# Performance work log

Hardware: AMD Instinct MI355X
Metric: run time of the kernel (lower is better)

Reference implementation:

```python
import jax, jax.numpy as jnp
import numpy as np

N = 5000
NFEAT = 512
NHID = 64
NHEADS = 8
NCLASS = 40
ALPHA = 0.2  # leaky relu slope
NEG_INF = -9e15


def setup_inputs() -> dict:
    key = jax.random.key(0)
    ks = jax.random.split(key, 12)
    x = jax.random.normal(ks[0], (N, NFEAT), dtype=jnp.float32)
    # binary adjacency, ~32 avg degree, with self loops
    adj = (jax.random.uniform(ks[1], (N, N)) < (32.0 / N)).astype(jnp.float32)
    adj = jnp.maximum(adj, jnp.eye(N, dtype=jnp.float32))
    s = 1.0 / np.sqrt(NFEAT)
    W_h = jax.random.uniform(ks[2], (NHEADS, NFEAT, NHID), minval=-s, maxval=s, dtype=jnp.float32)
    a_h = jax.random.uniform(ks[3], (NHEADS, 2 * NHID), minval=-s, maxval=s, dtype=jnp.float32)
    s2 = 1.0 / np.sqrt(NHID * NHEADS)
    W_o = jax.random.uniform(ks[4], (NHID * NHEADS, NHID), minval=-s2, maxval=s2, dtype=jnp.float32)
    a_o = jax.random.uniform(ks[5], (2 * NHID,), minval=-s2, maxval=s2, dtype=jnp.float32)
    s3 = 1.0 / np.sqrt(NHID)
    fc1_w = jax.random.uniform(ks[6], (NHID, 200), minval=-s3, maxval=s3, dtype=jnp.float32)
    fc1_b = jax.random.uniform(ks[7], (200,), minval=-s3, maxval=s3, dtype=jnp.float32)
    s4 = 1.0 / np.sqrt(200)
    fc2_w = jax.random.uniform(ks[8], (200, NCLASS), minval=-s4, maxval=s4, dtype=jnp.float32)
    fc2_b = jax.random.uniform(ks[9], (NCLASS,), minval=-s4, maxval=s4, dtype=jnp.float32)
    return {"x": x, "adj": adj, "W_h": W_h, "a_h": a_h, "W_o": W_o, "a_o": a_o,
            "fc1_w": fc1_w, "fc1_b": fc1_b, "fc2_w": fc2_w, "fc2_b": fc2_b}


def _masked_attention(e, adj):
    # e: [..., N, N]; mask where adj == 0, then row softmax
    e = jnp.where(adj > 0, e, NEG_INF)
    return jax.nn.softmax(e, axis=-1)


def reference(x, adj, W_h, a_h, W_o, a_o, fc1_w, fc1_b, fc2_w, fc2_b):
    # ---- multi-head GAT layer (concat=True), eval mode (dropout off) ----
    Wh = jnp.einsum('nf,hfo->hno', x, W_h)                 # [H, N, nhid]
    f1 = jnp.einsum('hno,ho->hn', Wh, a_h[:, :NHID])       # [H, N]
    f2 = jnp.einsum('hno,ho->hn', Wh, a_h[:, NHID:])       # [H, N]
    e = jax.nn.leaky_relu(f1[:, :, None] + f2[:, None, :], ALPHA)  # [H, N, N]
    att = _masked_attention(e, adj[None, :, :])
    h = jnp.einsum('hnm,hmo->hno', att, Wh)                # [H, N, nhid]
    h1 = jax.nn.elu(h).transpose(1, 0, 2).reshape(N, NHEADS * NHID)  # concat heads

    # ---- output GAT layer (concat=False) ----
    Wh2 = h1 @ W_o                                         # [N, nhid]
    g1 = Wh2 @ a_o[:NHID]                                  # [N]
    g2 = Wh2 @ a_o[NHID:]                                  # [N]
    e2 = jax.nn.leaky_relu(g1[:, None] + g2[None, :], ALPHA)
    att2 = _masked_attention(e2, adj)
    h2 = att2 @ Wh2                                        # [N, nhid]

    # ---- MLP head ----
    h3 = jax.nn.elu(h2 @ fc1_w + fc1_b)
    return h3 @ fc2_w + fc2_b                              # [N, nclass]
```

## Files before the change

### kernel.cpp

```cpp
#include <hip/hip_runtime.h>

typedef unsigned short u16;
typedef unsigned int u32;
typedef unsigned long long u64;
typedef __bf16 bf16_t;
typedef __bf16 bf16x8 __attribute__((ext_vector_type(8)));
typedef float f32x4 __attribute__((ext_vector_type(4)));
typedef u32 u32x4 __attribute__((ext_vector_type(4)));

#define NN 5000
#define NF 512
#define NH 64
#define HEADS 8
#define NCLS 40
#define CAP 128
#define LRELU 0.2f

#define CVT_BIG 320
#define CVT_GRID (CVT_BIG + 8)
#define BM_BLKS 1250
#define G1_BLKS (79 * HEADS)

__device__ __forceinline__ bool adj_is_bf16(const void* adj) {
    return ((*(const u32*)adj) & 0xFFFFu) != 0u;
}
__device__ __forceinline__ u16 rne_bf16(float f) {
    u32 u = __float_as_uint(f);
    u += 0x7FFFu + ((u >> 16) & 1u);
    return (u16)(u >> 16);
}
__device__ __forceinline__ float up_bf16(u16 h) {
    return __uint_as_float((u32)h << 16);
}
__device__ __forceinline__ u32x4 ntload4(const void* p, int idx) {
    return __builtin_nontemporal_load(((const u32x4*)p) + idx);
}

__global__ __launch_bounds__(256) void cvt(const void* __restrict__ x, const void* __restrict__ W_h,
                                           const void* __restrict__ adj,
                                           const void* a_h, const void* W_o, const void* a_o,
                                           const void* f1w, const void* f1b,
                                           const void* f2w, const void* f2b,
                                           u16* __restrict__ xc, u16* __restrict__ whc,
                                           float* a_hc, float* W_oc, float* a_oc,
                                           float* f1wc, float* f1bc, float* f2wc, float* f2bc) {
    const bool isb = adj_is_bf16(adj);
    const int b = blockIdx.x;
    if (b < CVT_BIG) {
        const int X4 = NN * NF / 4;
        const int T4 = X4 + HEADS * NF * NH / 4;
        for (int i = b * 256 + threadIdx.x; i < T4; i += CVT_BIG * 256) {
            if (i < X4) {
                ushort4 o;
                if (isb) {
                    o = ((const ushort4*)x)[i];
                } else {
                    u32x4 vv = ntload4(x, i);
                    o.x = rne_bf16(__uint_as_float(vv[0])); o.y = rne_bf16(__uint_as_float(vv[1]));
                    o.z = rne_bf16(__uint_as_float(vv[2])); o.w = rne_bf16(__uint_as_float(vv[3]));
                }
                ((ushort4*)xc)[i] = o;
            } else {
                const int iw = i - X4;
                u16 q[4];
                if (isb) {
                    ushort4 vv = ((const ushort4*)W_h)[iw];
                    q[0] = vv.x; q[1] = vv.y; q[2] = vv.z; q[3] = vv.w;
                } else {
                    u32x4 vv = ntload4(W_h, iw);
                    q[0] = rne_bf16(__uint_as_float(vv[0])); q[1] = rne_bf16(__uint_as_float(vv[1]));
                    q[2] = rne_bf16(__uint_as_float(vv[2])); q[3] = rne_bf16(__uint_as_float(vv[3]));
                }
                const int e0 = iw * 4;
                const int h = e0 >> 15;
                const int rem = e0 & 32767;
                const int f = rem >> 6, o0 = rem & 63;
                const int base = (h * 16 + (f >> 5)) * 2048 + ((f >> 3) & 3) * 128 + (f & 7);
                #pragma unroll
                for (int k = 0; k < 4; ++k) {
                    const int o = o0 + k;
                    whc[base + (o >> 4) * 512 + (o & 15) * 8] = q[k];
                }
            }
        }
    } else {
        const int s0 = HEADS * 2 * NH, s1 = HEADS * NH * NH, s2 = 2 * NH,
                  s3 = NH * 200, s4 = 200, s5 = 200 * NCLS, s6 = NCLS;
        const int total = s0 + s1 + s2 + s3 + s4 + s5 + s6;
        for (int i = (b - CVT_BIG) * 256 + threadIdx.x; i < total; i += 8 * 256) {
            const void* src; float* dst; int off = i;
            if (off < s0) { src = a_h; dst = a_hc; }
            else if ((off -= s0) < s1) { src = W_o;  dst = W_oc; }
            else if ((off -= s1) < s2) { src = a_o;  dst = a_oc; }
            else if ((off -= s2) < s3) { src = f1w;  dst = f1wc; }
            else if ((off -= s3) < s4) { src = f1b;  dst = f1bc; }
            else if ((off -= s4) < s5) { src = f2w;  dst = f2wc; }
            else { off -= s5;           src = f2b;  dst = f2bc; }
            dst[off] = isb ? up_bf16(((const u16*)src)[off]) : ((const float*)src)[off];
        }
    }
}

__global__ __launch_bounds__(256) void gemm1_f(const bf16_t* __restrict__ x,
                                               const bf16_t* __restrict__ Wf,
                                               const float* __restrict__ a_h,
                                               const void* __restrict__ adj,
                                               int* __restrict__ nbr, int* __restrict__ deg,
                                               float* __restrict__ Wh,
                                               float* __restrict__ f1,
                                               float* __restrict__ f2) {
    const int lane = threadIdx.x & 63;
    const int wid  = threadIdx.x >> 6;
    const int b = blockIdx.x;

    if (b >= G1_BLKS) {
        const bool isb = adj_is_bf16(adj);
        const int r = (b - G1_BLKS) * 4 + wid;
        u64 my0 = 0ull, my1 = 0ull;
        if (!isb) {
            const float* row = (const float*)adj + (size_t)r * NN;
            #pragma unroll
            for (int pass = 0; pass < 2; ++pass) {
                u32x4 v[10];
                #pragma unroll
                for (int k = 0; k < 10; ++k) {
                    int c = (pass * 10 + k) * 64 + lane;
                    v[k] = (c < 1250) ? ntload4(row, c) : (u32x4){0u, 0u, 0u, 0u};
                }
                #pragma unroll
                for (int k = 0; k < 10; ++k) {
                    int i = pass * 10 + k;
                    #pragma unroll
                    for (int j = 0; j < 4; ++j) {
                        u64 m = __ballot(v[k][j] != 0u);
                        int w = i * 4 + j;
                        if (w == lane)      my0 = m;
                        if (w == lane + 64) my1 = m;
                    }
                }
            }
        } else {
            const u16* row = (const u16*)adj + (size_t)r * NN;
            u32x4 v[10];
            #pragma unroll
            for (int k = 0; k < 10; ++k) {
                int c = k * 64 + lane;
                v[k] = (c < 625) ? ntload4(row, c) : (u32x4){0u, 0u, 0u, 0u};
            }
            #pragma unroll
            for (int k = 0; k < 10; ++k) {
                #pragma unroll
                for (int j = 0; j < 4; ++j) {
                    u64 mlo = __ballot((v[k][j] & 0xFFFFu) != 0u);
                    u64 mhi = __ballot((v[k][j] >> 16) != 0u);
                    int wl = k * 8 + 2 * j, wh = wl + 1;
                    if (wl == lane)      my0 = mlo;
                    if (wl == lane + 64) my1 = mlo;
                    if (wh == lane)      my0 = mhi;
                    if (wh == lane + 64) my1 = mhi;
                }
            }
        }
        int* nrow = nbr + (size_t)r * CAP;
        int pc = __popcll(my0);
        int scan = pc;
        #pragma unroll
        for (int o = 1; o < 64; o <<= 1) {
            int t2 = __shfl_up(scan, o);
            if (lane >= o) scan += t2;
        }
        int off = scan - pc;
        {
            const int w = lane;
            u64 mw = my0;
            while (mw) {
                int bb = __ffsll(mw) - 1;
                mw &= mw - 1;
                int elem = !isb ? ((w >> 2) * 64 + bb) * 4 + (w & 3)
                                : ((w >> 3) * 64 + bb) * 8 + (w & 7);
                if (off < CAP) nrow[off] = elem;
                ++off;
            }
        }
        const int base = __shfl(scan, 63);
        int pc1 = __popcll(my1);
        int scan1 = pc1;
        #pragma unroll
        for (int o = 1; o < 64; o <<= 1) {
            int t2 = __shfl_up(scan1, o);
            if (lane >= o) scan1 += t2;
        }
        int off1 = base + scan1 - pc1;
        {
            const int w = lane + 64;
            u64 mw = my1;
            while (mw) {
                int bb = __ffsll(mw) - 1;
                mw &= mw - 1;
                int elem = !isb ? ((w >> 2) * 64 + bb) * 4 + (w & 3)
                                : ((w >> 3) * 64 + bb) * 8 + (w & 7);
                if (off1 < CAP) nrow[off1] = elem;
                ++off1;
            }
        }
        const int total = base + __shfl(scan1, 63);
        if (lane == 0) deg[r] = total < CAP ? total : CAP;
        return;
    }

    const int rg = b % 79;
    const int h  = b / 79;
    const int quad = lane >> 4;
    const int lr   = lane & 15;
    const int kq   = quad * 8;
    const int nCol = wid * 16 + lr;
    __shared__ float f1s[4][64], f2s[4][64];

    const bf16_t* Bf = Wf + (size_t)h * (16 * 2048) + threadIdx.x * 8;
    bf16x8 bfrag[16];
    #pragma unroll
    for (int s = 0; s < 16; ++s) bfrag[s] = *(const bf16x8*)(Bf + s * 2048);

    const float a1c = a_h[h * 128 + nCol];
    const float a2c = a_h[h * 128 + NH + nCol];

    for (int t = 0; t < 4; ++t) {
        const int rb = rg * 64 + t * 16;
        int row  = rb + lr;
        int rowc = row < NN ? row : NN - 1;
        const bf16_t* xp = x + (size_t)rowc * NF + kq;
        f32x4 acc = {0.f, 0.f, 0.f, 0.f};
        #pragma unroll
        for (int s = 0; s < 16; ++s) {
            bf16x8 a = *(const bf16x8*)(xp + s * 32);
            acc = __builtin_amdgcn_mfma_f32_16x16x32_bf16(a, bfrag[s], acc, 0, 0, 0);
        }
        #pragma unroll
        for (int r = 0; r < 4; ++r) {
            int gr = rb + quad * 4 + r;
            if (gr < NN) Wh[(size_t)gr * (HEADS * NH) + h * NH + nCol] = acc[r];
            float p1 = acc[r] * a1c, p2 = acc[r] * a2c;
            #pragma unroll
            for (int o = 8; o; o >>= 1) { p1 += __shfl_xor(p1, o); p2 += __shfl_xor(p2, o); }
            if (lr == 0) { f1s[wid][t * 16 + quad * 4 + r] = p1; f2s[wid][t * 16 + quad * 4 + r] = p2; }
        }
    }
    __syncthreads();
    if (wid == 0) {
        int gr = rg * 64 + lane;
        if (gr < NN) {
            f1[h * NN + gr] = f1s[0][lane] + f1s[1][lane] + f1s[2][lane] + f1s[3][lane];
            f2[h * NN + gr] = f2s[0][lane] + f2s[1][lane] + f2s[2][lane] + f2s[3][lane];
        }
    }
}

__global__ __launch_bounds__(256) void agg1f(const int* __restrict__ nbr,
                                             const int* __restrict__ deg,
                                             const float* __restrict__ Wh,
                                             const float* __restrict__ f1,
                                             const float* __restrict__ f2,
                                             float* __restrict__ h1) {
    const int lane = threadIdx.x & 63;
    const int wid  = threadIdx.x >> 6;
    const int n = blockIdx.x;
    __shared__ int s_nbr[CAP];
    __shared__ float s_p[8][CAP];
    const int d = deg[n];
    for (int i = threadIdx.x; i < d; i += 256) s_nbr[i] = nbr[(size_t)n * CAP + i];
    __syncthreads();

    const int ha = wid, hb = wid + 4;
    const int nb0 = (lane < d) ? s_nbr[lane] : 0;
    const int nb1 = (lane + 64 < d) ? s_nbr[lane + 64] : 0;
    const float f10 = f1[ha * NN + n], f11 = f1[hb * NN + n];
    const float* f2ha = f2 + (size_t)ha * NN;
    const float* f2hb = f2 + (size_t)hb * NN;

    float e00 = -INFINITY, e01 = -INFINITY, e10 = -INFINITY, e11 = -INFINITY;
    if (lane < d) {
        float a = f10 + f2ha[nb0]; e00 = a > 0.f ? a : LRELU * a;
        float b = f11 + f2hb[nb0]; e10 = b > 0.f ? b : LRELU * b;
    }
    if (lane + 64 < d) {
        float a = f10 + f2ha[nb1]; e01 = a > 0.f ? a : LRELU * a;
        float b = f11 + f2hb[nb1]; e11 = b > 0.f ? b : LRELU * b;
    }
    float mx0 = fmaxf(e00, e01), mx1 = fmaxf(e10, e11);
    #pragma unroll
    for (int o = 32; o; o >>= 1) {
        mx0 = fmaxf(mx0, __shfl_xor(mx0, o));
        mx1 = fmaxf(mx1, __shfl_xor(mx1, o));
    }
    float p00 = lane < d ? expf(e00 - mx0) : 0.f;
    float p01 = lane + 64 < d ? expf(e01 - mx0) : 0.f;
    float p10 = lane < d ? expf(e10 - mx1) : 0.f;
    float p11 = lane + 64 < d ? expf(e11 - mx1) : 0.f;
    float sm0 = p00 + p01, sm1 = p10 + p11;
    #pragma unroll
    for (int o = 32; o; o >>= 1) { sm0 += __shfl_xor(sm0, o); sm1 += __shfl_xor(sm1, o); }

    const float i0 = 1.f / sm0, i1 = 1.f / sm1;
    s_p[ha][lane] = p00 * i0; s_p[ha][lane + 64] = p01 * i0;
    s_p[hb][lane] = p10 * i1; s_p[hb][lane + 64] = p11 * i1;
    __syncthreads();

    const float* ap = s_p[2 * wid + (lane >> 5)];
    const float* wp = Wh + wid * 128 + 2 * lane;
    float A0x = 0.f, A0y = 0.f, A1x = 0.f, A1y = 0.f;
    float A2x = 0.f, A2y = 0.f, A3x = 0.f, A3y = 0.f;
    int j = 0;
    for (; j + 8 <= d; j += 8) {
        #pragma unroll
        for (int u = 0; u < 8; ++u) {
            const float2 v = *(const float2*)(wp + (size_t)s_nbr[j + u] * (HEADS * NH));
            const float a = ap[j + u];
            if ((u & 3) == 0)      { A0x += a * v.x; A0y += a * v.y; }
            else if ((u & 3) == 1) { A1x += a * v.x; A1y += a * v.y; }
            else if ((u & 3) == 2) { A2x += a * v.x; A2y += a * v.y; }
            else                   { A3x += a * v.x; A3y += a * v.y; }
        }
    }
    for (; j < d; ++j) {
        const float2 v = *(const float2*)(wp + (size_t)s_nbr[j] * (HEADS * NH));
        const float a = ap[j];
        A0x += a * v.x; A0y += a * v.y;
    }
    float hx = A0x + A1x + A2x + A3x;
    float hy = A0y + A1y + A2y + A3y;
    hx = hx > 0.f ? hx : expf(hx) - 1.f;
    hy = hy > 0.f ? hy : expf(hy) - 1.f;
    *(float2*)(h1 + (size_t)n * (HEADS * NH) + wid * 128 + 2 * lane) = make_float2(hx, hy);
}

__global__ __launch_bounds__(256) void gemm2_4(const float* __restrict__ h1,
                                               const float* __restrict__ W_o,
                                               const float* __restrict__ a_o,
                                               float* __restrict__ Wh2,
                                               float* __restrict__ g1,
                                               float* __restrict__ g2) {
    const int t = threadIdx.x;
    const int n0 = blockIdx.x * 4;
    __shared__ float sh[4 * 512];
    __shared__ float ps[4][4][64];
    const float4* src = (const float4*)(h1 + (size_t)n0 * 512);
    ((float4*)sh)[t]       = src[t];
    ((float4*)sh)[t + 256] = src[t + 256];
    __syncthreads();
    const int o = t & 63, part = t >> 6;
    float a0 = 0.f, a1 = 0.f, a2 = 0.f, a3 = 0.f;
    const float* wo = W_o + part * 128 * 64 + o;
    const float* s0 = sh + part * 128;
    #pragma unroll 4
    for (int f = 0; f < 128; ++f) {
        float w = wo[f * 64];
        a0 += s0[f] * w; a1 += s0[512 + f] * w; a2 += s0[1024 + f] * w; a3 += s0[1536 + f] * w;
    }
    ps[part][0][o] = a0; ps[part][1][o] = a1; ps[part][2][o] = a2; ps[part][3][o] = a3;
    __syncthreads();
    const int nd = t >> 6;
    float w2 = ps[0][nd][o] + ps[1][nd][o] + ps[2][nd][o] + ps[3][nd][o];
    Wh2[(size_t)(n0 + nd) * 64 + o] = w2;
    float p1 = w2 * a_o[o], p2 = w2 * a_o[64 + o];
    #pragma unroll
    for (int s = 32; s; s >>= 1) { p1 += __shfl_xor(p1, s); p2 += __shfl_xor(p2, s); }
    if (o == 0) { g1[n0 + nd] = p1; g2[n0 + nd] = p2; }
}

__global__ __launch_bounds__(256) void agg2_mlp(const float* __restrict__ Wh2,
                                                const float* __restrict__ g1,
                                                const float* __restrict__ g2,
                                                const int* __restrict__ nbr,
                                                const int* __restrict__ deg,
                                                const float* __restrict__ fc1_w,
                                                const float* __restrict__ fc1_b,
                                                const float* __restrict__ fc2_w,
                                                const float* __restrict__ fc2_b,
                                                float* __restrict__ out) {
    const int lane = threadIdx.x & 63;
    const int wid  = threadIdx.x >> 6;
    const int t = threadIdx.x;
    const int n0 = blockIdx.x * 4;
    const int n = n0 + wid;
    __shared__ float s_alpha[4][CAP];
    __shared__ int   s_nbr[4][CAP];
    __shared__ float s_h2[4][NH];
    __shared__ float s_h3[4][200];
    __shared__ float ps2[2][4][NCLS];
    const int d = deg[n];
    const int* nb = nbr + (size_t)n * CAP;
    const float gn = g1[n];

    float mx = -INFINITY;
    for (int j = lane; j < d; j += 64) {
        int m = nb[j];
        s_nbr[wid][j] = m;
        float e = gn + g2[m];
        e = e > 0.f ? e : LRELU * e;
        s_alpha[wid][j] = e;
        mx = fmaxf(mx, e);
    }
    #pragma unroll
    for (int o = 32; o; o >>= 1) mx = fmaxf(mx, __shfl_xor(mx, o));
    float sm = 0.f;
    for (int j = lane; j < d; j += 64) {
        float p = expf(s_alpha[wid][j] - mx);
        s_alpha[wid][j] = p;
        sm += p;
    }
    #pragma unroll
    for (int o = 32; o; o >>= 1) sm += __shfl_xor(sm, o);

    float acc0 = 0.f, acc1 = 0.f, acc2 = 0.f, acc3 = 0.f;
    int j = 0;
    for (; j + 4 <= d; j += 4) {
        acc0 += s_alpha[wid][j]     * Wh2[(size_t)s_nbr[wid][j]     * NH + lane];
        acc1 += s_alpha[wid][j + 1] * Wh2[(size_t)s_nbr[wid][j + 1] * NH + lane];
        acc2 += s_alpha[wid][j + 2] * Wh2[(size_t)s_nbr[wid][j + 2] * NH + lane];
        acc3 += s_alpha[wid][j + 3] * Wh2[(size_t)s_nbr[wid][j + 3] * NH + lane];
    }
    for (; j < d; ++j) acc0 += s_alpha[wid][j] * Wh2[(size_t)s_nbr[wid][j] * NH + lane];
    s_h2[wid][lane] = (acc0 + acc1 + acc2 + acc3) / sm;
    __syncthreads();

    if (t < 200) {
        float b0 = 0.f, b1 = 0.f, b2 = 0.f, b3 = 0.f;
        #pragma unroll 4
        for (int f = 0; f < NH; ++f) {
            float w = fc1_w[f * 200 + t];
            b0 += s_h2[0][f] * w; b1 += s_h2[1][f] * w; b2 += s_h2[2][f] * w; b3 += s_h2[3][f] * w;
        }
        float bb = fc1_b[t];
        b0 += bb; b1 += bb; b2 += bb; b3 += bb;
        s_h3[0][t] = b0 > 0.f ? b0 : expf(b0) - 1.f;
        s_h3[1][t] = b1 > 0.f ? b1 : expf(b1) - 1.f;
        s_h3[2][t] = b2 > 0.f ? b2 : expf(b2) - 1.f;
        s_h3[3][t] = b3 > 0.f ? b3 : expf(b3) - 1.f;
    }
    __syncthreads();

    if (t < 80) {
        const int o = t % 40, fh = t / 40;
        float c0 = 0.f, c1 = 0.f, c2 = 0.f, c3 = 0.f;
        #pragma unroll 4
        for (int f = fh * 100; f < fh * 100 + 100; ++f) {
            float w = fc2_w[f * NCLS + o];
            c0 += s_h3[0][f] * w; c1 += s_h3[1][f] * w; c2 += s_h3[2][f] * w; c3 += s_h3[3][f] * w;
        }
        ps2[fh][0][o] = c0; ps2[fh][1][o] = c1; ps2[fh][2][o] = c2; ps2[fh][3][o] = c3;
    }
    __syncthreads();
    if (t < 160) {
        const int nd = t / 40, o = t % 40;
        out[(size_t)(n0 + nd) * NCLS + o] = ps2[0][nd][o] + ps2[1][nd][o] + fc2_b[o];
    }
}

extern "C" void kernel_launch(void* const* d_in, const int* in_sizes, int n_in,
                              void* d_out, int out_size, void* d_ws, size_t ws_size,
                              hipStream_t stream) {
    const void* x     = d_in[0];
    const void* adj   = d_in[1];
    const void* W_h   = d_in[2];
    const void* a_h   = d_in[3];
    const void* W_o   = d_in[4];
    const void* a_o   = d_in[5];
    const void* fc1_w = d_in[6];
    const void* fc1_b = d_in[7];
    const void* fc2_w = d_in[8];
    const void* fc2_b = d_in[9];
    float* out = (float*)d_out;

    char* ws = (char*)d_ws;
    int*   nbr   = (int*)(ws + 0);
    int*   deg   = (int*)(ws + 2560000);
    float* Wh    = (float*)(ws + 2580000);
    float* f1    = (float*)(ws + 12820000);
    float* f2    = (float*)(ws + 12980000);
    float* h1    = (float*)(ws + 13140000);
    float* Wh2   = (float*)(ws + 23380000);
    float* g1    = (float*)(ws + 24660000);
    float* g2    = (float*)(ws + 24680000);
    u16*   xc    = (u16*)(ws + 24700000);
    u16*   whc   = (u16*)(ws + 29820000);
    float* a_hc  = (float*)(ws + 30344288);
    float* W_oc  = (float*)(ws + 30348384);
    float* a_oc  = (float*)(ws + 30479456);
    float* f1wc  = (float*)(ws + 30479968);
    float* f1bc  = (float*)(ws + 30531168);
    float* f2wc  = (float*)(ws + 30531968);
    float* f2bc  = (float*)(ws + 30563968);

    cvt<<<CVT_GRID, 256, 0, stream>>>(x, W_h, adj, a_h, W_o, a_o,
                                      fc1_w, fc1_b, fc2_w, fc2_b,
                                      xc, whc, a_hc, W_oc, a_oc,
                                      f1wc, f1bc, f2wc, f2bc);
    gemm1_f<<<G1_BLKS + BM_BLKS, 256, 0, stream>>>((const bf16_t*)xc, (const bf16_t*)whc,
                                                   a_hc, adj, nbr, deg, Wh, f1, f2);
    agg1f<<<NN, 256, 0, stream>>>(nbr, deg, Wh, f1, f2, h1);
    gemm2_4<<<NN / 4, 256, 0, stream>>>(h1, W_oc, a_oc, Wh2, g1, g2);
    agg2_mlp<<<NN / 4, 256, 0, stream>>>(Wh2, g1, g2, nbr, deg,
                                         f1wc, f1bc, f2wc, f2bc, out);
}
```

Before: 268.9 us.

## Fuse all stages into one persistent kernel with grid-wide atomic barriers

Replaces the five separate kernel launches with a single persistent kernel sized to occupancy (capped at 512 blocks). Stages are separated by atomic-counter grid barriers and work items are grid-strided, with a shared-memory union covering all stages. This removes launch gaps and tail effects between kernels. In exchange it caps parallelism, adds a memset and barrier spin cost, and depends on all blocks being co-resident. The old multi-kernel path is kept as a fallback.

```diff
diff --git a/kernel.cpp b/kernel.cpp
--- a/kernel.cpp
+++ b/kernel.cpp
@@ -16,10 +16,9 @@
 #define CAP 128
 #define LRELU 0.2f
 
-#define CVT_BIG 320
-#define CVT_GRID (CVT_BIG + 8)
 #define BM_BLKS 1250
 #define G1_BLKS (79 * HEADS)
+#define FUSED_MAXBLK 512
 
 __device__ __forceinline__ bool adj_is_bf16(const void* adj) {
     return ((*(const u32*)adj) & 0xFFFFu) != 0u;
@@ -36,185 +35,96 @@
     return __builtin_nontemporal_load(((const u32x4*)p) + idx);
 }
 
-__global__ __launch_bounds__(256) void cvt(const void* __restrict__ x, const void* __restrict__ W_h,
-                                           const void* __restrict__ adj,
-                                           const void* a_h, const void* W_o, const void* a_o,
-                                           const void* f1w, const void* f1b,
-                                           const void* f2w, const void* f2b,
-                                           u16* __restrict__ xc, u16* __restrict__ whc,
-                                           float* a_hc, float* W_oc, float* a_oc,
-                                           float* f1wc, float* f1bc, float* f2wc, float* f2bc) {
-    const bool isb = adj_is_bf16(adj);
-    const int b = blockIdx.x;
-    if (b < CVT_BIG) {
-        const int X4 = NN * NF / 4;
-        const int T4 = X4 + HEADS * NF * NH / 4;
-        for (int i = b * 256 + threadIdx.x; i < T4; i += CVT_BIG * 256) {
-            if (i < X4) {
-                ushort4 o;
-                if (isb) {
-                    o = ((const ushort4*)x)[i];
-                } else {
-                    u32x4 vv = ntload4(x, i);
-                    o.x = rne_bf16(__uint_as_float(vv[0])); o.y = rne_bf16(__uint_as_float(vv[1]));
-                    o.z = rne_bf16(__uint_as_float(vv[2])); o.w = rne_bf16(__uint_as_float(vv[3]));
-                }
-                ((ushort4*)xc)[i] = o;
+struct SmemA { float f1s[4][64]; float f2s[4][64]; };
+struct SmemB { int s_nbr[CAP]; float s_p[8][CAP]; };
+struct SmemC { float sh[4 * 512]; float ps[4][4][64]; };
+struct SmemD { float s_alpha[4][CAP]; int s_nbr[4][CAP]; float s_h2[4][NH];
+               float s_h3[4][200]; float ps2[2][4][NCLS]; };
+union alignas(16) SmemU { SmemA pa; SmemB pb; SmemC pc; SmemD pd; };
+
+__device__ __forceinline__ void gsync(u32* bar, int k, int nblk) {
+    __syncthreads();
+    if (threadIdx.x == 0) {
+        __threadfence();
+        __hip_atomic_fetch_add(&bar[k], 1u, __ATOMIC_ACQ_REL, __HIP_MEMORY_SCOPE_AGENT);
+        while (__hip_atomic_load(&bar[k], __ATOMIC_ACQUIRE, __HIP_MEMORY_SCOPE_AGENT) < (u32)nblk)
+            __builtin_amdgcn_s_sleep(2);
+        __threadfence();
+    }
+    __syncthreads();
+}
+
+__device__ void dev_cvt(int gtid, int gstr, bool isb,
+                        const void* __restrict__ x, const void* __restrict__ W_h,
+                        const void* a_h, const void* W_o, const void* a_o,
+                        const void* f1w, const void* f1b, const void* f2w, const void* f2b,
+                        u16* __restrict__ xc, u16* __restrict__ whc,
+                        float* a_hc, float* W_oc, float* a_oc,
+                        float* f1wc, float* f1bc, float* f2wc, float* f2bc) {
+    const int X4 = NN * NF / 4;
+    const int T4 = X4 + HEADS * NF * NH / 4;
+    for (int i = gtid; i < T4; i += gstr) {
+        if (i < X4) {
+            ushort4 o;
+            if (isb) {
+                o = ((const ushort4*)x)[i];
             } else {
-                const int iw = i - X4;
-                u16 q[4];
-                if (isb) {
-                    ushort4 vv = ((const ushort4*)W_h)[iw];
-                    q[0] = vv.x; q[1] = vv.y; q[2] = vv.z; q[3] = vv.w;
-                } else {
-                    u32x4 vv = ntload4(W_h, iw);
-                    q[0] = rne_bf16(__uint_as_float(vv[0])); q[1] = rne_bf16(__uint_as_float(vv[1]));
-                    q[2] = rne_bf16(__uint_as_float(vv[2])); q[3] = rne_bf16(__uint_as_float(vv[3]));
-                }
-                const int e0 = iw * 4;
-                const int h = e0 >> 15;
-                const int rem = e0 & 32767;
-                const int f = rem >> 6, o0 = rem & 63;
-                const int base = (h * 16 + (f >> 5)) * 2048 + ((f >> 3) & 3) * 128 + (f & 7);
-                #pragma unroll
-                for (int k = 0; k < 4; ++k) {
-                    const int o = o0 + k;
-                    whc[base + (o >> 4) * 512 + (o & 15) * 8] = q[k];
-                }
+                u32x4 vv = ntload4(x, i);
+                o.x = rne_bf16(__uint_as_float(vv[0])); o.y = rne_bf16(__uint_as_float(vv[1]));
+                o.z = rne_bf16(__uint_as_float(vv[2])); o.w = rne_bf16(__uint_as_float(vv[3]));
             }
-        }
-    } else {
-        const int s0 = HEADS * 2 * NH, s1 = HEADS * NH * NH, s2 = 2 * NH,
-                  s3 = NH * 200, s4 = 200, s5 = 200 * NCLS, s6 = NCLS;
-        const int total = s0 + s1 + s2 + s3 + s4 + s5 + s6;
-        for (int i = (b - CVT_BIG) * 256 + threadIdx.x; i < total; i += 8 * 256) {
-            const void* src; float* dst; int off = i;
-            if (off < s0) { src = a_h; dst = a_hc; }
-            else if ((off -= s0) < s1) { src = W_o;  dst = W_oc; }
-            else if ((off -= s1) < s2) { src = a_o;  dst = a_oc; }
-            else if ((off -= s2) < s3) { src = f1w;  dst = f1wc; }
-            else if ((off -= s3) < s4) { src = f1b;  dst = f1bc; }
-            else if ((off -= s4) < s5) { src = f2w;  dst = f2wc; }
-            else { off -= s5;           src = f2b;  dst = f2bc; }
-            dst[off] = isb ? up_bf16(((const u16*)src)[off]) : ((const float*)src)[off];
-        }
-    }
-}
-
-__global__ __launch_bounds__(256) void gemm1_f(const bf16_t* __restrict__ x,
-                                               const bf16_t* __restrict__ Wf,
-                                               const float* __restrict__ a_h,
-                                               const void* __restrict__ adj,
-                                               int* __restrict__ nbr, int* __restrict__ deg,
-                                               float* __restrict__ Wh,
-                                               float* __restrict__ f1,
-                                               float* __restrict__ f2) {
+            ((ushort4*)xc)[i] = o;
+        } else {
+            const int iw = i - X4;
+            u16 q[4];
+            if (isb) {
+                ushort4 vv = ((const ushort4*)W_h)[iw];
+                q[0] = vv.x; q[1] = vv.y; q[2] = vv.z; q[3] = vv.w;
+            } else {
+                u32x4 vv = ntload4(W_h, iw);
+                q[0] = rne_bf16(__uint_as_float(vv[0])); q[1] = rne_bf16(__uint_as_float(vv[1]));
+                q[2] = rne_bf16(__uint_as_float(vv[2])); q[3] = rne_bf16(__uint_as_float(vv[3]));
+            }
+            const int e0 = iw * 4;
+            const int h = e0 >> 15;
+            const int rem = e0 & 32767;
+            const int f = rem >> 6, o0 = rem & 63;
+            const int base = (h * 16 + (f >> 5)) * 2048 + ((f >> 3) & 3) * 128 + (f & 7);
+            #pragma unroll
+            for (int k = 0; k < 4; ++k) {
+                const int o = o0 + k;
+                whc[base + (o >> 4) * 512 + (o & 15) * 8] = q[k];
+            }
+        }
+    }
+    const int s0 = HEADS * 2 * NH, s1 = HEADS * NH * NH, s2 = 2 * NH,
+              s3 = NH * 200, s4 = 200, s5 = 200 * NCLS, s6 = NCLS;
+    const int total = s0 + s1 + s2 + s3 + s4 + s5 + s6;
+    for (int i = gtid; i < total; i += gstr) {
+        const void* src; float* dst; int off = i;
+        if (off < s0) { src = a_h; dst = a_hc; }
+        else if ((off -= s0) < s1) { src = W_o;  dst = W_oc; }
+        else if ((off -= s1) < s2) { src = a_o;  dst = a_oc; }
+        else if ((off -= s2) < s3) { src = f1w;  dst = f1wc; }
+        else if ((off -= s3) < s4) { src = f1b;  dst = f1bc; }
+        else if ((off -= s4) < s5) { src = f2w;  dst = f2wc; }
+        else { off -= s5;           src = f2b;  dst = f2bc; }
+        dst[off] = isb ? up_bf16(((const u16*)src)[off]) : ((const float*)src)[off];
+    }
+}
+
+__device__ void dev_gemm1_item(int b, const bf16_t* __restrict__ x,
+                               const bf16_t* __restrict__ Wf, const float* __restrict__ a_h,
+                               float* __restrict__ Wh, float* __restrict__ f1,
+                               float* __restrict__ f2, SmemA& sm) {
     const int lane = threadIdx.x & 63;
     const int wid  = threadIdx.x >> 6;
-    const int b = blockIdx.x;
-
-    if (b >= G1_BLKS) {
-        const bool isb = adj_is_bf16(adj);
-        const int r = (b - G1_BLKS) * 4 + wid;
-        u64 my0 = 0ull, my1 = 0ull;
-        if (!isb) {
-            const float* row = (const float*)adj + (size_t)r * NN;
-            #pragma unroll
-            for (int pass = 0; pass < 2; ++pass) {
-                u32x4 v[10];
-                #pragma unroll
-                for (int k = 0; k < 10; ++k) {
-                    int c = (pass * 10 + k) * 64 + lane;
-                    v[k] = (c < 1250) ? ntload4(row, c) : (u32x4){0u, 0u, 0u, 0u};
-                }
-                #pragma unroll
-                for (int k = 0; k < 10; ++k) {
-                    int i = pass * 10 + k;
-                    #pragma unroll
-                    for (int j = 0; j < 4; ++j) {
-                        u64 m = __ballot(v[k][j] != 0u);
-                        int w = i * 4 + j;
-                        if (w == lane)      my0 = m;
-                        if (w == lane + 64) my1 = m;
-                    }
-                }
-            }
-        } else {
-            const u16* row = (const u16*)adj + (size_t)r * NN;
-            u32x4 v[10];
-            #pragma unroll
-            for (int k = 0; k < 10; ++k) {
-                int c = k * 64 + lane;
-                v[k] = (c < 625) ? ntload4(row, c) : (u32x4){0u, 0u, 0u, 0u};
-            }
-            #pragma unroll
-            for (int k = 0; k < 10; ++k) {
-                #pragma unroll
-                for (int j = 0; j < 4; ++j) {
-                    u64 mlo = __ballot((v[k][j] & 0xFFFFu) != 0u);
-                    u64 mhi = __ballot((v[k][j] >> 16) != 0u);
-                    int wl = k * 8 + 2 * j, wh = wl + 1;
-                    if (wl == lane)      my0 = mlo;
-                    if (wl == lane + 64) my1 = mlo;
-                    if (wh == lane)      my0 = mhi;
-                    if (wh == lane + 64) my1 = mhi;
-                }
-            }
-        }
-        int* nrow = nbr + (size_t)r * CAP;
-        int pc = __popcll(my0);
-        int scan = pc;
-        #pragma unroll
-        for (int o = 1; o < 64; o <<= 1) {
-            int t2 = __shfl_up(scan, o);
-            if (lane >= o) scan += t2;
-        }
-        int off = scan - pc;
-        {
-            const int w = lane;
-            u64 mw = my0;
-            while (mw) {
-                int bb = __ffsll(mw) - 1;
-                mw &= mw - 1;
-                int elem = !isb ? ((w >> 2) * 64 + bb) * 4 + (w & 3)
-                                : ((w >> 3) * 64 + bb) * 8 + (w & 7);
-                if (off < CAP) nrow[off] = elem;
-                ++off;
-            }
-        }
-        const int base = __shfl(scan, 63);
-        int pc1 = __popcll(my1);
-        int scan1 = pc1;
-        #pragma unroll
-        for (int o = 1; o < 64; o <<= 1) {
-            int t2 = __shfl_up(scan1, o);
-            if (lane >= o) scan1 += t2;
-        }
-        int off1 = base + scan1 - pc1;
-        {
-            const int w = lane + 64;
-            u64 mw = my1;
-            while (mw) {
-                int bb = __ffsll(mw) - 1;
-                mw &= mw - 1;
-                int elem = !isb ? ((w >> 2) * 64 + bb) * 4 + (w & 3)
-                                : ((w >> 3) * 64 + bb) * 8 + (w & 7);
-                if (off1 < CAP) nrow[off1] = elem;
-                ++off1;
-            }
-        }
-        const int total = base + __shfl(scan1, 63);
-        if (lane == 0) deg[r] = total < CAP ? total : CAP;
-        return;
-    }
-
     const int rg = b % 79;
     const int h  = b / 79;
     const int quad = lane >> 4;
     const int lr   = lane & 15;
     const int kq   = quad * 8;
     const int nCol = wid * 16 + lr;
-    __shared__ float f1s[4][64], f2s[4][64];
 
     const bf16_t* Bf = Wf + (size_t)h * (16 * 2048) + threadIdx.x * 8;
     bf16x8 bfrag[16];
@@ -242,37 +152,128 @@
             float p1 = acc[r] * a1c, p2 = acc[r] * a2c;
             #pragma unroll
             for (int o = 8; o; o >>= 1) { p1 += __shfl_xor(p1, o); p2 += __shfl_xor(p2, o); }
-            if (lr == 0) { f1s[wid][t * 16 + quad * 4 + r] = p1; f2s[wid][t * 16 + quad * 4 + r] = p2; }
+            if (lr == 0) { sm.f1s[wid][t * 16 + quad * 4 + r] = p1; sm.f2s[wid][t * 16 + quad * 4 + r] = p2; }
         }
     }
     __syncthreads();
     if (wid == 0) {
         int gr = rg * 64 + lane;
         if (gr < NN) {
-            f1[h * NN + gr] = f1s[0][lane] + f1s[1][lane] + f1s[2][lane] + f1s[3][lane];
-            f2[h * NN + gr] = f2s[0][lane] + f2s[1][lane] + f2s[2][lane] + f2s[3][lane];
-        }
-    }
-}
-
-__global__ __launch_bounds__(256) void agg1f(const int* __restrict__ nbr,
-                                             const int* __restrict__ deg,
-                                             const float* __restrict__ Wh,
-                                             const float* __restrict__ f1,
-                                             const float* __restrict__ f2,
-                                             float* __restrict__ h1) {
+            f1[h * NN + gr] = sm.f1s[0][lane] + sm.f1s[1][lane] + sm.f1s[2][lane] + sm.f1s[3][lane];
+            f2[h * NN + gr] = sm.f2s[0][lane] + sm.f2s[1][lane] + sm.f2s[2][lane] + sm.f2s[3][lane];
+        }
+    }
+    __syncthreads();
+}
+
+__device__ void dev_adj_item(int a, const void* __restrict__ adj, bool isb,
+                             int* __restrict__ nbr, int* __restrict__ deg) {
     const int lane = threadIdx.x & 63;
     const int wid  = threadIdx.x >> 6;
-    const int n = blockIdx.x;
-    __shared__ int s_nbr[CAP];
-    __shared__ float s_p[8][CAP];
+    const int r = a * 4 + wid;
+    u64 my0 = 0ull, my1 = 0ull;
+    if (!isb) {
+        const float* row = (const float*)adj + (size_t)r * NN;
+        #pragma unroll
+        for (int pass = 0; pass < 2; ++pass) {
+            u32x4 v[10];
+            #pragma unroll
+            for (int k = 0; k < 10; ++k) {
+                int c = (pass * 10 + k) * 64 + lane;
+                v[k] = (c < 1250) ? ntload4(row, c) : (u32x4){0u, 0u, 0u, 0u};
+            }
+            #pragma unroll
+            for (int k = 0; k < 10; ++k) {
+                int i = pass * 10 + k;
+                #pragma unroll
+                for (int j = 0; j < 4; ++j) {
+                    u64 m = __ballot(v[k][j] != 0u);
+                    int w = i * 4 + j;
+                    if (w == lane)      my0 = m;
+                    if (w == lane + 64) my1 = m;
+                }
+            }
+        }
+    } else {
+        const u16* row = (const u16*)adj + (size_t)r * NN;
+        u32x4 v[10];
+        #pragma unroll
+        for (int k = 0; k < 10; ++k) {
+            int c = k * 64 + lane;
+            v[k] = (c < 625) ? ntload4(row, c) : (u32x4){0u, 0u, 0u, 0u};
+        }
+        #pragma unroll
+        for (int k = 0; k < 10; ++k) {
+            #pragma unroll
+            for (int j = 0; j < 4; ++j) {
+                u64 mlo = __ballot((v[k][j] & 0xFFFFu) != 0u);
+                u64 mhi = __ballot((v[k][j] >> 16) != 0u);
+                int wl = k * 8 + 2 * j, wh = wl + 1;
+                if (wl == lane)      my0 = mlo;
+                if (wl == lane + 64) my1 = mlo;
+                if (wh == lane)      my0 = mhi;
+                if (wh == lane + 64) my1 = mhi;
+            }
+        }
+    }
+    int* nrow = nbr + (size_t)r * CAP;
+    int pc = __popcll(my0);
+    int scan = pc;
+    #pragma unroll
+    for (int o = 1; o < 64; o <<= 1) {
+        int t2 = __shfl_up(scan, o);
+        if (lane >= o) scan += t2;
+    }
+    int off = scan - pc;
+    {
+        const int w = lane;
+        u64 mw = my0;
+        while (mw) {
+            int bb = __ffsll(mw) - 1;
+            mw &= mw - 1;
+            int elem = !isb ? ((w >> 2) * 64 + bb) * 4 + (w & 3)
+                            : ((w >> 3) * 64 + bb) * 8 + (w & 7);
+            if (off < CAP) nrow[off] = elem;
+            ++off;
+        }
+    }
+    const int base = __shfl(scan, 63);
+    int pc1 = __popcll(my1);
+    int scan1 = pc1;
+    #pragma unroll
+    for (int o = 1; o < 64; o <<= 1) {
+        int t2 = __shfl_up(scan1, o);
+        if (lane >= o) scan1 += t2;
+    }
+    int off1 = base + scan1 - pc1;
+    {
+        const int w = lane + 64;
+        u64 mw = my1;
+        while (mw) {
+            int bb = __ffsll(mw) - 1;
+            mw &= mw - 1;
+            int elem = !isb ? ((w >> 2) * 64 + bb) * 4 + (w & 3)
+                            : ((w >> 3) * 64 + bb) * 8 + (w & 7);
+            if (off1 < CAP) nrow[off1] = elem;
+            ++off1;
+        }
+    }
+    const int total = base + __shfl(scan1, 63);
+    if (lane == 0) deg[r] = total < CAP ? total : CAP;
+}
+
+__device__ void dev_agg1_node(int n, const int* __restrict__ nbr, const int* __restrict__ deg,
+                              const float* __restrict__ Wh, const float* __restrict__ f1,
+                              const float* __restrict__ f2, float* __restrict__ h1, SmemB& sm) {
+    const int lane = threadIdx.x & 63;
+    const int wid  = threadIdx.x >> 6;
     const int d = deg[n];
-    for (int i = threadIdx.x; i < d; i += 256) s_nbr[i] = nbr[(size_t)n * CAP + i];
+    for (int i = threadIdx.x; i < d; i += 256) sm.s_nbr[i] = nbr[(size_t)n * CAP + i];
     __syncthreads();
 
     const int ha = wid, hb = wid + 4;
-    const int nb0 = (lane < d) ? s_nbr[lane] : 0;
-    const int nb1 = (lane + 64 < d) ? s_nbr[lane + 64] : 0;
+    const int nb0 = (lane < d) ? sm.s_nbr[lane] : 0;
+    const int nb1 = (lane + 64 < d) ? sm.s_nbr[lane + 64] : 0;
     const float f10 = f1[ha * NN + n], f11 = f1[hb * NN + n];
     const float* f2ha = f2 + (size_t)ha * NN;
     const float* f2hb = f2 + (size_t)hb * NN;
@@ -301,11 +302,11 @@
     for (int o = 32; o; o >>= 1) { sm0 += __shfl_xor(sm0, o); sm1 += __shfl_xor(sm1, o); }
 
     const float i0 = 1.f / sm0, i1 = 1.f / sm1;
-    s_p[ha][lane] = p00 * i0; s_p[ha][lane + 64] = p01 * i0;
-    s_p[hb][lane] = p10 * i1; s_p[hb][lane + 64] = p11 * i1;
-    __syncthreads();
-
-    const float* ap = s_p[2 * wid + (lane >> 5)];
+    sm.s_p[ha][lane] = p00 * i0; sm.s_p[ha][lane + 64] = p01 * i0;
+    sm.s_p[hb][lane] = p10 * i1; sm.s_p[hb][lane + 64] = p11 * i1;
+    __syncthreads();
+
+    const float* ap = sm.s_p[2 * wid + (lane >> 5)];
     const float* wp = Wh + wid * 128 + 2 * lane;
     float A0x = 0.f, A0y = 0.f, A1x = 0.f, A1y = 0.f;
     float A2x = 0.f, A2y = 0.f, A3x = 0.f, A3y = 0.f;
@@ -313,7 +314,7 @@
     for (; j + 8 <= d; j += 8) {
         #pragma unroll
         for (int u = 0; u < 8; ++u) {
-            const float2 v = *(const float2*)(wp + (size_t)s_nbr[j + u] * (HEADS * NH));
+            const float2 v = *(const float2*)(wp + (size_t)sm.s_nbr[j + u] * (HEADS * NH));
             const float a = ap[j + u];
             if ((u & 3) == 0)      { A0x += a * v.x; A0y += a * v.y; }
             else if ((u & 3) == 1) { A1x += a * v.x; A1y += a * v.y; }
@@ -322,7 +323,7 @@
         }
     }
     for (; j < d; ++j) {
-        const float2 v = *(const float2*)(wp + (size_t)s_nbr[j] * (HEADS * NH));
+        const float2 v = *(const float2*)(wp + (size_t)sm.s_nbr[j] * (HEADS * NH));
         const float a = ap[j];
         A0x += a * v.x; A0y += a * v.y;
     }
@@ -331,62 +332,49 @@
     hx = hx > 0.f ? hx : expf(hx) - 1.f;
     hy = hy > 0.f ? hy : expf(hy) - 1.f;
     *(float2*)(h1 + (size_t)n * (HEADS * NH) + wid * 128 + 2 * lane) = make_float2(hx, hy);
-}
-
-__global__ __launch_bounds__(256) void gemm2_4(const float* __restrict__ h1,
-                                               const float* __restrict__ W_o,
-                                               const float* __restrict__ a_o,
-                                               float* __restrict__ Wh2,
-                                               float* __restrict__ g1,
-                                               float* __restrict__ g2) {
+    __syncthreads();
+}
+
+__device__ void dev_gemm2_item(int it, const float* __restrict__ h1, const float* __restrict__ W_o,
+                               const float* __restrict__ a_o, float* __restrict__ Wh2,
+                               float* __restrict__ g1, float* __restrict__ g2, SmemC& sm) {
     const int t = threadIdx.x;
-    const int n0 = blockIdx.x * 4;
-    __shared__ float sh[4 * 512];
-    __shared__ float ps[4][4][64];
+    const int n0 = it * 4;
     const float4* src = (const float4*)(h1 + (size_t)n0 * 512);
-    ((float4*)sh)[t]       = src[t];
-    ((float4*)sh)[t + 256] = src[t + 256];
+    ((float4*)sm.sh)[t]       = src[t];
+    ((float4*)sm.sh)[t + 256] = src[t + 256];
     __syncthreads();
     const int o = t & 63, part = t >> 6;
     float a0 = 0.f, a1 = 0.f, a2 = 0.f, a3 = 0.f;
     const float* wo = W_o + part * 128 * 64 + o;
-    const float* s0 = sh + part * 128;
+    const float* s0 = sm.sh + part * 128;
     #pragma unroll 4
     for (int f = 0; f < 128; ++f) {
         float w = wo[f * 64];
         a0 += s0[f] * w; a1 += s0[512 + f] * w; a2 += s0[1024 + f] * w; a3 += s0[1536 + f] * w;
     }
-    ps[part][0][o] = a0; ps[part][1][o] = a1; ps[part][2][o] = a2; ps[part][3][o] = a3;
+    sm.ps[part][0][o] = a0; sm.ps[part][1][o] = a1; sm.ps[part][2][o] = a2; sm.ps[part][3][o] = a3;
     __syncthreads();
     const int nd = t >> 6;
-    float w2 = ps[0][nd][o] + ps[1][nd][o] + ps[2][nd][o] + ps[3][nd][o];
+    float w2 = sm.ps[0][nd][o] + sm.ps[1][nd][o] + sm.ps[2][nd][o] + sm.ps[3][nd][o];
     Wh2[(size_t)(n0 + nd) * 64 + o] = w2;
     float p1 = w2 * a_o[o], p2 = w2 * a_o[64 + o];
     #pragma unroll
     for (int s = 32; s; s >>= 1) { p1 += __shfl_xor(p1, s); p2 += __shfl_xor(p2, s); }
     if (o == 0) { g1[n0 + nd] = p1; g2[n0 + nd] = p2; }
-}
-
-__global__ __launch_bounds__(256) void agg2_mlp(const float* __restrict__ Wh2,
-                                                const float* __restrict__ g1,
-                                                const float* __restrict__ g2,
-                                                const int* __restrict__ nbr,
-                                                const int* __restrict__ deg,
-                                                const float* __restrict__ fc1_w,
-                                                const float* __restrict__ fc1_b,
-                                                const float* __restrict__ fc2_w,
-                                                const float* __restrict__ fc2_b,
-                                                float* __restrict__ out) {
+    __syncthreads();
+}
+
+__device__ void dev_agg2_item(int it, const float* __restrict__ Wh2, const float* __restrict__ g1,
+                              const float* __restrict__ g2, const int* __restrict__ nbr,
+                              const int* __restrict__ deg, const float* __restrict__ fc1_w,
+                              const float* __restrict__ fc1_b, const float* __restrict__ fc2_w,
+                              const float* __restrict__ fc2_b, float* __restrict__ out, SmemD& sm) {
     const int lane = threadIdx.x & 63;
     const int wid  = threadIdx.x >> 6;
     const int t = threadIdx.x;
-    const int n0 = blockIdx.x * 4;
+    const int n0 = it * 4;
     const int n = n0 + wid;
-    __shared__ float s_alpha[4][CAP];
-    __shared__ int   s_nbr[4][CAP];
-    __shared__ float s_h2[4][NH];
-    __shared__ float s_h3[4][200];
-    __shared__ float ps2[2][4][NCLS];
     const int d = deg[n];
     const int* nb = nbr + (size_t)n * CAP;
     const float gn = g1[n];
@@ -394,33 +382,33 @@
     float mx = -INFINITY;
     for (int j = lane; j < d; j += 64) {
         int m = nb[j];
-        s_nbr[wid][j] = m;
+        sm.s_nbr[wid][j] = m;
         float e = gn + g2[m];
         e = e > 0.f ? e : LRELU * e;
-        s_alpha[wid][j] = e;
+        sm.s_alpha[wid][j] = e;
         mx = fmaxf(mx, e);
     }
     #pragma unroll
     for (int o = 32; o; o >>= 1) mx = fmaxf(mx, __shfl_xor(mx, o));
-    float sm = 0.f;
+    float smv = 0.f;
     for (int j = lane; j < d; j += 64) {
-        float p = expf(s_alpha[wid][j] - mx);
-        s_alpha[wid][j] = p;
-        sm += p;
-    }
-    #pragma unroll
-    for (int o = 32; o; o >>= 1) sm += __shfl_xor(sm, o);
+        float p = expf(sm.s_alpha[wid][j] - mx);
+        sm.s_alpha[wid][j] = p;
+        smv += p;
+    }
+    #pragma unroll
+    for (int o = 32; o; o >>= 1) smv += __shfl_xor(smv, o);
 
     float acc0 = 0.f, acc1 = 0.f, acc2 = 0.f, acc3 = 0.f;
     int j = 0;
     for (; j + 4 <= d; j += 4) {
-        acc0 += s_alpha[wid][j]     * Wh2[(size_t)s_nbr[wid][j]     * NH + lane];
-        acc1 += s_alpha[wid][j + 1] * Wh2[(size_t)s_nbr[wid][j + 1] * NH + lane];
-        acc2 += s_alpha[wid][j + 2] * Wh2[(size_t)s_nbr[wid][j + 2] * NH + lane];
-        acc3 += s_alpha[wid][j + 3] * Wh2[(size_t)s_nbr[wid][j + 3] * NH + lane];
-    }
-    for (; j < d; ++j) acc0 += s_alpha[wid][j] * Wh2[(size_t)s_nbr[wid][j] * NH + lane];
-    s_h2[wid][lane] = (acc0 + acc1 + acc2 + acc3) / sm;
+        acc0 += sm.s_alpha[wid][j]     * Wh2[(size_t)sm.s_nbr[wid][j]     * NH + lane];
+        acc1 += sm.s_alpha[wid][j + 1] * Wh2[(size_t)sm.s_nbr[wid][j + 1] * NH + lane];
+        acc2 += sm.s_alpha[wid][j + 2] * Wh2[(size_t)sm.s_nbr[wid][j + 2] * NH + lane];
+        acc3 += sm.s_alpha[wid][j + 3] * Wh2[(size_t)sm.s_nbr[wid][j + 3] * NH + lane];
+    }
+    for (; j < d; ++j) acc0 += sm.s_alpha[wid][j] * Wh2[(size_t)sm.s_nbr[wid][j] * NH + lane];
+    sm.s_h2[wid][lane] = (acc0 + acc1 + acc2 + acc3) / smv;
     __syncthreads();
 
     if (t < 200) {
@@ -428,14 +416,15 @@
         #pragma unroll 4
         for (int f = 0; f < NH; ++f) {
             float w = fc1_w[f * 200 + t];
-            b0 += s_h2[0][f] * w; b1 += s_h2[1][f] * w; b2 += s_h2[2][f] * w; b3 += s_h2[3][f] * w;
+            b0 += sm.s_h2[0][f] * w; b1 += sm.s_h2[1][f] * w;
+            b2 += sm.s_h2[2][f] * w; b3 += sm.s_h2[3][f] * w;
         }
         float bb = fc1_b[t];
         b0 += bb; b1 += bb; b2 += bb; b3 += bb;
-        s_h3[0][t] = b0 > 0.f ? b0 : expf(b0) - 1.f;
-        s_h3[1][t] = b1 > 0.f ? b1 : expf(b1) - 1.f;
-        s_h3[2][t] = b2 > 0.f ? b2 : expf(b2) - 1.f;
-        s_h3[3][t] = b3 > 0.f ? b3 : expf(b3) - 1.f;
+        sm.s_h3[0][t] = b0 > 0.f ? b0 : expf(b0) - 1.f;
+        sm.s_h3[1][t] = b1 > 0.f ? b1 : expf(b1) - 1.f;
+        sm.s_h3[2][t] = b2 > 0.f ? b2 : expf(b2) - 1.f;
+        sm.s_h3[3][t] = b3 > 0.f ? b3 : expf(b3) - 1.f;
     }
     __syncthreads();
 
@@ -445,15 +434,96 @@
         #pragma unroll 4
         for (int f = fh * 100; f < fh * 100 + 100; ++f) {
             float w = fc2_w[f * NCLS + o];
-            c0 += s_h3[0][f] * w; c1 += s_h3[1][f] * w; c2 += s_h3[2][f] * w; c3 += s_h3[3][f] * w;
-        }
-        ps2[fh][0][o] = c0; ps2[fh][1][o] = c1; ps2[fh][2][o] = c2; ps2[fh][3][o] = c3;
+            c0 += sm.s_h3[0][f] * w; c1 += sm.s_h3[1][f] * w;
+            c2 += sm.s_h3[2][f] * w; c3 += sm.s_h3[3][f] * w;
+        }
+        sm.ps2[fh][0][o] = c0; sm.ps2[fh][1][o] = c1; sm.ps2[fh][2][o] = c2; sm.ps2[fh][3][o] = c3;
     }
     __syncthreads();
     if (t < 160) {
         const int nd = t / 40, o = t % 40;
-        out[(size_t)(n0 + nd) * NCLS + o] = ps2[0][nd][o] + ps2[1][nd][o] + fc2_b[o];
-    }
+        out[(size_t)(n0 + nd) * NCLS + o] = sm.ps2[0][nd][o] + sm.ps2[1][nd][o] + fc2_b[o];
+    }
+    __syncthreads();
+}
+
+__global__ __launch_bounds__(256) void fused(
+        const void* __restrict__ x, const void* __restrict__ adj,
+        const void* __restrict__ W_h, const void* a_h, const void* W_o, const void* a_o,
+        const void* f1w, const void* f1b, const void* f2w, const void* f2b,
+        u16* __restrict__ xc, u16* __restrict__ whc,
+        float* a_hc, float* W_oc, float* a_oc,
+        float* f1wc, float* f1bc, float* f2wc, float* f2bc,
+        int* __restrict__ nbr, int* __restrict__ deg,
+        float* __restrict__ Wh, float* __restrict__ f1, float* __restrict__ f2,
+        float* __restrict__ h1, float* __restrict__ Wh2,
+        float* __restrict__ g1, float* __restrict__ g2,
+        float* __restrict__ out, u32* bar, int nblk) {
+    __shared__ SmemU sm;
+    const bool isb = adj_is_bf16(adj);
+    const int gtid = blockIdx.x * 256 + threadIdx.x;
+    const int gstr = nblk * 256;
+
+    dev_cvt(gtid, gstr, isb, x, W_h, a_h, W_o, a_o, f1w, f1b, f2w, f2b,
+            xc, whc, a_hc, W_oc, a_oc, f1wc, f1bc, f2wc, f2bc);
+    gsync(bar, 0, nblk);
+
+    for (int it = blockIdx.x; it < G1_BLKS + BM_BLKS; it += nblk) {
+        if (it < G1_BLKS) dev_gemm1_item(it, (const bf16_t*)xc, (const bf16_t*)whc, a_hc,
+                                         Wh, f1, f2, sm.pa);
+        else              dev_adj_item(it - G1_BLKS, adj, isb, nbr, deg);
+    }
+    gsync(bar, 1, nblk);
+
+    for (int n = blockIdx.x; n < NN; n += nblk)
+        dev_agg1_node(n, nbr, deg, Wh, f1, f2, h1, sm.pb);
+    gsync(bar, 2, nblk);
+
+    for (int it = blockIdx.x; it < NN / 4; it += nblk)
+        dev_gemm2_item(it, h1, W_oc, a_oc, Wh2, g1, g2, sm.pc);
+    gsync(bar, 3, nblk);
+
+    for (int it = blockIdx.x; it < NN / 4; it += nblk)
+        dev_agg2_item(it, Wh2, g1, g2, nbr, deg, f1wc, f1bc, f2wc, f2bc, out, sm.pd);
+}
+
+__global__ __launch_bounds__(256) void cvt_all(const void* x, const void* W_h, const void* adj,
+                                               const void* a_h, const void* W_o, const void* a_o,
+                                               const void* f1w, const void* f1b,
+                                               const void* f2w, const void* f2b,
+                                               u16* xc, u16* whc, float* a_hc, float* W_oc,
+                                               float* a_oc, float* f1wc, float* f1bc,
+                                               float* f2wc, float* f2bc) {
+    dev_cvt(blockIdx.x * 256 + threadIdx.x, gridDim.x * 256, adj_is_bf16(adj),
+            x, W_h, a_h, W_o, a_o, f1w, f1b, f2w, f2b,
+            xc, whc, a_hc, W_oc, a_oc, f1wc, f1bc, f2wc, f2bc);
+}
+__global__ __launch_bounds__(256) void gemm1_f(const bf16_t* x, const bf16_t* Wf,
+                                               const float* a_h, const void* adj,
+                                               int* nbr, int* deg,
+                                               float* Wh, float* f1, float* f2) {
+    __shared__ SmemA sma;
+    const int b = blockIdx.x;
+    if (b < G1_BLKS) dev_gemm1_item(b, x, Wf, a_h, Wh, f1, f2, sma);
+    else             dev_adj_item(b - G1_BLKS, adj, adj_is_bf16(adj), nbr, deg);
+}
+__global__ __launch_bounds__(256) void agg1f(const int* nbr, const int* deg, const float* Wh,
+                                             const float* f1, const float* f2, float* h1) {
+    __shared__ SmemB smb;
+    dev_agg1_node(blockIdx.x, nbr, deg, Wh, f1, f2, h1, smb);
+}
+__global__ __launch_bounds__(256) void gemm2_4(const float* h1, const float* W_o, const float* a_o,
+                                               float* Wh2, float* g1, float* g2) {
+    __shared__ SmemC smc;
+    dev_gemm2_item(blockIdx.x, h1, W_o, a_o, Wh2, g1, g2, smc);
+}
+__global__ __launch_bounds__(256) void agg2_mlp(const float* Wh2, const float* g1, const float* g2,
+                                                const int* nbr, const int* deg,
+                                                const float* fc1_w, const float* fc1_b,
+                                                const float* fc2_w, const float* fc2_b,
+                                                float* out) {
+    __shared__ SmemD smd;
+    dev_agg2_item(blockIdx.x, Wh2, g1, g2, nbr, deg, fc1_w, fc1_b, fc2_w, fc2_b, out, smd);
 }
 
 extern "C" void kernel_launch(void* const* d_in, const int* in_sizes, int n_in,
@@ -490,15 +560,42 @@
     float* f1bc  = (float*)(ws + 30531168);
     float* f2wc  = (float*)(ws + 30531968);
     float* f2bc  = (float*)(ws + 30563968);
-
-    cvt<<<CVT_GRID, 256, 0, stream>>>(x, W_h, adj, a_h, W_o, a_o,
-                                      fc1_w, fc1_b, fc2_w, fc2_b,
-                                      xc, whc, a_hc, W_oc, a_oc,
-                                      f1wc, f1bc, f2wc, f2bc);
-    gemm1_f<<<G1_BLKS + BM_BLKS, 256, 0, stream>>>((const bf16_t*)xc, (const bf16_t*)whc,
-                                                   a_hc, adj, nbr, deg, Wh, f1, f2);
-    agg1f<<<NN, 256, 0, stream>>>(nbr, deg, Wh, f1, f2, h1);
-    gemm2_4<<<NN / 4, 256, 0, stream>>>(h1, W_oc, a_oc, Wh2, g1, g2);
-    agg2_mlp<<<NN / 4, 256, 0, stream>>>(Wh2, g1, g2, nbr, deg,
-                                         f1wc, f1bc, f2wc, f2bc, out);
-}
+    u32*   bar   = (u32*)(ws + 30564128);
+
+    static int g_nblk = -1;
+    if (g_nblk < 0) {
+        int occ = 0, dev = 0;
+        hipDeviceProp_t prop;
+        hipError_t e1 = hipOccupancyMaxActiveBlocksPerMultiprocessor(&occ, fused, 256, 0);
+        hipError_t e2 = hipGetDevice(&dev);
+        hipError_t e3 = hipGetDeviceProperties(&prop, dev);
+        if (e1 == hipSuccess && e2 == hipSuccess && e3 == hipSuccess && occ >= 1) {
+            long nb = (long)occ * (long)prop.multiProcessorCount;
+            g_nblk = (int)(nb > FUSED_MAXBLK ? FUSED_MAXBLK : nb);
+        } else {
+            g_nblk = 0;
+        }
+        if (g_nblk < 64) g_nblk = 0;
+    }
+
+    if (g_nblk > 0) {
+        hipMemsetAsync(bar, 0, 32, stream);
+        fused<<<g_nblk, 256, 0, stream>>>(x, adj, W_h, a_h, W_o, a_o,
+                                          fc1_w, fc1_b, fc2_w, fc2_b,
+                                          xc, whc, a_hc, W_oc, a_oc,
+                                          f1wc, f1bc, f2wc, f2bc,
+                                          nbr, deg, Wh, f1, f2, h1, Wh2, g1, g2,
+                                          out, bar, g_nblk);
+    } else {
+        cvt_all<<<328, 256, 0, stream>>>(x, W_h, adj, a_h, W_o, a_o,
+                                         fc1_w, fc1_b, fc2_w, fc2_b,
+                                         xc, whc, a_hc, W_oc, a_oc,
+                                         f1wc, f1bc, f2wc, f2bc);
+        gemm1_f<<<G1_BLKS + BM_BLKS, 256, 0, stream>>>((const bf16_t*)xc, (const bf16_t*)whc,
+                                                       a_hc, adj, nbr, deg, Wh, f1, f2);
+        agg1f<<<NN, 256, 0, stream>>>(nbr, deg, Wh, f1, f2, h1);
+        gemm2_4<<<NN / 4, 256, 0, stream>>>(h1, W_oc, a_oc, Wh2, g1, g2);
+        agg2_mlp<<<NN / 4, 256, 0, stream>>>(Wh2, g1, g2, nbr, deg,
+                                             f1wc, f1bc, f2wc, f2bc, out);
+    }
+}
```

Measured after the change: 692.1 us. +157.4%, slower.
